# Kernel tuning notes

Hardware: AMD Instinct MI355X
Metric: run time of the kernel (lower is better)

The kernel has to match this reference:

```python
import jax, jax.numpy as jnp
import numpy as np

HEAD_SIZE = 64
EMBED = 512


def setup_inputs() -> dict:
    key = jax.random.key(0)
    kx, kk, kq, kv = jax.random.split(key, 4)
    x = jax.random.normal(kx, (4, 4096, EMBED), dtype=jnp.float32)
    # torch Linear(EMBED, HEAD_SIZE, bias=False) weight: [HEAD_SIZE, EMBED]
    scale = 1.0 / np.sqrt(EMBED)
    Wk = jax.random.normal(kk, (HEAD_SIZE, EMBED), dtype=jnp.float32) * scale
    Wq = jax.random.normal(kq, (HEAD_SIZE, EMBED), dtype=jnp.float32) * scale
    Wv = jax.random.normal(kv, (HEAD_SIZE, EMBED), dtype=jnp.float32) * scale
    return {"x": x, "Wk": Wk, "Wq": Wq, "Wv": Wv}


def reference(x, Wk, Wq, Wv):
    B, T, C = x.shape
    # projections: x @ W.T  -> [B, T, H]
    k = jnp.einsum('btc,hc->bth', x, Wk)
    q = jnp.einsum('btc,hc->bth', x, Wq)
    v = jnp.einsum('btc,hc->bth', x, Wv)
    # scores scaled by C**-0.5 (input embed dim, as in the source module)
    scores = jnp.einsum('bth,bsh->bts', q, k) * (C ** -0.5)  # [B, T, T]
    causal = jnp.tril(jnp.ones((T, T), dtype=bool))
    scores = jnp.where(causal, scores, -jnp.inf)
    weights = jax.nn.softmax(scores, axis=-1)
    # dropout p=0.0 -> identity
    out = jnp.einsum('bts,bsh->bth', weights, v)  # [B, T, H]
    return out
```

## Files before the change

kernel.cpp:

```cpp
#include <hip/hip_runtime.h>

typedef unsigned short u16;
typedef unsigned int   u32;

#define NB 4
#define NT 4096
#define NC 512
#define NH 64
#define ATT_SCALE 0.044194173824159216f
#define LOG2E     1.4426950408889634f
#define QSCALE    (ATT_SCALE * LOG2E)
#define NEG_BIG   -30000.0f
#define ITEMS3_PB 288

typedef __attribute__((ext_vector_type(8))) _Float16 half8;
typedef __attribute__((ext_vector_type(4))) _Float16 half4;
typedef __attribute__((ext_vector_type(4))) float    floatx4;

__device__ __forceinline__ void gload_lds16(const _Float16* g, _Float16* l) {
    __builtin_amdgcn_global_load_lds(
        (const __attribute__((address_space(1))) void*)g,
        (__attribute__((address_space(3))) void*)l, 16, 0, 0);
}


__global__ __launch_bounds__(256) void wconv(
    const float* __restrict__ Wk, const float* __restrict__ Wq,
    const float* __restrict__ Wv, _Float16* __restrict__ Wh)
{
    const int gid = blockIdx.x * 256 + threadIdx.x;
    const int w = gid >> 13;
    const int i = gid & 8191;
    const int h = i >> 7, c = (i & 127) * 4;
    const float* src = (w == 0) ? Wq : (w == 1) ? Wk : Wv;
    const float sc = (w == 0) ? QSCALE : 1.0f;
    float4 f = *(const float4*)&src[h * NC + c];
    half4 o = {(_Float16)(f.x * sc), (_Float16)(f.y * sc),
               (_Float16)(f.z * sc), (_Float16)(f.w * sc)};
    const int blk = ((w * 16 + (c >> 5)) * 4 + (h >> 4));
    *(half4*)&Wh[(size_t)blk * 512 + (h & 15) * 32 + ((c >> 3) & 3) * 8 + (c & 7)] = o;
}

__global__ __launch_bounds__(256) void qkv_mfma(
    const float* __restrict__ x, const _Float16* __restrict__ Wh,
    _Float16* __restrict__ Qf, _Float16* __restrict__ Kf,
    _Float16* __restrict__ Vf)
{
    __shared__ __align__(16) floatx4 red[3][12][64];

    const int tid  = threadIdx.x;
    const int wv   = tid >> 6;
    const int lane = tid & 63;
    const int quad = lane >> 4;
    const int id   = lane & 15;
    const int rowbase = blockIdx.x * 16;

    floatx4 acc[3][4] = {};
    const float* xp = x + (size_t)(rowbase + id) * NC + wv * 128;
    const int loff = id * 32 + quad * 8;

    float4 xr[8];
#pragma unroll
    for (int ksq = 0; ksq < 8; ++ksq)
        xr[ksq] = *(const float4*)&xp[(ksq >> 1) * 32 + quad * 8 + (ksq & 1) * 4];

#pragma unroll
    for (int ks = 0; ks < 4; ++ks) {
        float4 f0 = xr[2 * ks];
        float4 f1 = xr[2 * ks + 1];
        half8 a;
        a[0] = (_Float16)f0.x; a[1] = (_Float16)f0.y;
        a[2] = (_Float16)f0.z; a[3] = (_Float16)f0.w;
        a[4] = (_Float16)f1.x; a[5] = (_Float16)f1.y;
        a[6] = (_Float16)f1.z; a[7] = (_Float16)f1.w;
        const int ksg = wv * 4 + ks;
#pragma unroll
        for (int w = 0; w < 3; ++w)
#pragma unroll
            for (int nt = 0; nt < 4; ++nt) {
                half8 bf = *(const half8*)&Wh[(size_t)((w * 16 + ksg) * 4 + nt) * 512 + loff];
                acc[w][nt] = __builtin_amdgcn_mfma_f32_16x16x32_f16(a, bf, acc[w][nt], 0, 0, 0);
            }
    }

#pragma unroll
    for (int idx = 0; idx < 12; ++idx) {
        const int ow = idx / 3;
        if (ow != wv)
            red[(wv > ow) ? wv - 1 : wv][idx][lane] = acc[idx >> 2][idx & 3];
    }
    __syncthreads();

    const int b  = rowbase >> 12, L = rowbase & 4095;
    const int q16 = L >> 4, kt = L >> 6, tt = (L >> 4) & 3;
    const int kop = ((rowbase & 63) + quad * 4) >> 5;
    const int q4k = ((((rowbase & 63) + quad * 4) >> 3) & 3);

#define QKV_EPIL(IDX) do {                                                     \
    constexpr int w_ = (IDX) >> 2, nt_ = (IDX) & 3;                            \
    floatx4 a_ = acc[w_][nt_];                                                 \
    a_ += red[0][IDX][lane] + red[1][IDX][lane] + red[2][IDX][lane];           \
    if (w_ == 0 || w_ == 1) {                                                  \
        const int hop = nt_ >> 1;                                              \
        const int q4h = (nt_ * 2 + (id >> 3)) & 3;                             \
        const int j   = id & 7;                                                \
        const size_t ad = (w_ == 0)                                            \
            ? (size_t)((b * 256 + q16) * 2 + hop) * 512 + q4h * 8 + j          \
            : (size_t)(((b * 64 + kt) * 4 + tt) * 2 + hop) * 512 + q4h * 8 + j;\
        _Float16* dstp = (w_ == 0) ? Qf : Kf;                                  \
        _Pragma("unroll")                                                      \
        for (int r = 0; r < 4; ++r)                                            \
            dstp[ad + (quad * 4 + r) * 32] = (_Float16)a_[r];                  \
    } else {                                                                   \
        half4 vh = {(_Float16)a_[0], (_Float16)a_[1],                          \
                    (_Float16)a_[2], (_Float16)a_[3]};                         \
        const size_t va = (size_t)(((b * 64 + kt) * 4 + nt_) * 2 + kop) * 512  \
                        + id * 32 + q4k * 8 + (quad & 1) * 4;                  \
        *(half4*)&Vf[va] = vh;                                                 \
    }                                                                          \
} while (0)

    if (wv == 0)      { QKV_EPIL(0); QKV_EPIL(1);  QKV_EPIL(2);  }
    else if (wv == 1) { QKV_EPIL(3); QKV_EPIL(4);  QKV_EPIL(5);  }
    else if (wv == 2) { QKV_EPIL(6); QKV_EPIL(7);  QKV_EPIL(8);  }
    else              { QKV_EPIL(9); QKV_EPIL(10); QKV_EPIL(11); }
#undef QKV_EPIL
}

__global__ __launch_bounds__(256) void attn_part(
    const _Float16* __restrict__ Qf, const _Float16* __restrict__ Kf,
    const _Float16* __restrict__ Vf, _Float16* __restrict__ Opart,
    float2* __restrict__ MLpart)
{
    constexpr int KP = 72;
    __shared__ __align__(16) _Float16 KV[2][2][4096];
    __shared__ __align__(16) _Float16 Ps[4][16 * KP];

    const int tid  = threadIdx.x;
    const int wv   = tid >> 6;
    const int lane = tid & 63;
    const int quad = lane >> 4;
    const int id   = lane & 15;
    const int b    = blockIdx.y;
    const int item = (ITEMS3_PB - 1) - blockIdx.x;
    const int loff = id * 32 + quad * 8;

    int g = (int)(0.5f * (__builtin_sqrtf((float)item + 1.0f) - 1.0f));
    while (4 * (g + 1) * (g + 2) <= item) ++g;
    while (g > 0 && 4 * g * (g + 1) > item) --g;
    const int rem = item - 4 * g * (g + 1);
    const int np  = g + 1;
    const int qb  = 8 * g + rem / np;
    const int seg = rem - (rem / np) * np;
    const int ntl = qb + 1;
    const int t0 = seg * ntl / np, t1 = (seg + 1) * ntl / np;

    const size_t qa = (size_t)((b * 256 + qb * 4 + wv) * 2) * 512 + loff;
    const half8 qb0 = *(const half8*)&Qf[qa];
    const half8 qb1 = *(const half8*)&Qf[qa + 512];

    size_t gk = (size_t)((b * 64 + t0) * 8) * 512;
    const int c0 = 2 * wv, c1 = 2 * wv + 1;

    gload_lds16(&Kf[gk + (size_t)c0 * 512 + loff], &KV[0][0][c0 * 512]);
    gload_lds16(&Kf[gk + (size_t)c1 * 512 + loff], &KV[0][0][c1 * 512]);
    gload_lds16(&Vf[gk + (size_t)c0 * 512 + loff], &KV[0][1][c0 * 512]);
    gload_lds16(&Vf[gk + (size_t)c1 * 512 + loff], &KV[0][1][c1 * 512]);

    floatx4 o[4] = {};
    float m_i = NEG_BIG;
    float l_q = 0.f;

    asm volatile("s_waitcnt vmcnt(0)" ::: "memory");
    __syncthreads();

    int cur = 0;
    for (int kt = t0; kt < t1; ++kt) {
        const bool more = (kt + 1 < t1);
        if (more) {
            const size_t gn = gk + 4096;
            gload_lds16(&Kf[gn + (size_t)c0 * 512 + loff], &KV[cur ^ 1][0][c0 * 512]);
            gload_lds16(&Kf[gn + (size_t)c1 * 512 + loff], &KV[cur ^ 1][0][c1 * 512]);
            gload_lds16(&Vf[gn + (size_t)c0 * 512 + loff], &KV[cur ^ 1][1][c0 * 512]);
            gload_lds16(&Vf[gn + (size_t)c1 * 512 + loff], &KV[cur ^ 1][1][c1 * 512]);
        }
        const _Float16* Kc = &KV[cur][0][0];
        const _Float16* Vc = &KV[cur][1][0];

        floatx4 s4[4] = {};
#pragma unroll
        for (int t = 0; t < 4; ++t) {
            const half8 k0 = *(const half8*)&Kc[(size_t)(2 * t)     * 512 + lane * 8];
            const half8 k1 = *(const half8*)&Kc[(size_t)(2 * t + 1) * 512 + lane * 8];
            s4[t] = __builtin_amdgcn_mfma_f32_16x16x32_f16(k0, qb0, s4[t], 0, 0, 0);
            s4[t] = __builtin_amdgcn_mfma_f32_16x16x32_f16(k1, qb1, s4[t], 0, 0, 0);
        }

        if (kt == qb) {
            const int qrow = wv * 16 + id;
#pragma unroll
            for (int t = 0; t < 4; ++t)
#pragma unroll
                for (int r = 0; r < 4; ++r)
                    if (16 * t + quad * 4 + r > qrow)
                        s4[t][r] = NEG_BIG;
        }

        half8 vf[8];
#pragma unroll
        for (int c = 0; c < 8; ++c)
            vf[c] = *(const half8*)&Vc[(size_t)c * 512 + lane * 8];

        float pmax = s4[0][0];
#pragma unroll
        for (int t = 0; t < 4; ++t)
#pragma unroll
            for (int r = 0; r < 4; ++r) pmax = fmaxf(pmax, s4[t][r]);

        if (__any(pmax > m_i + 8.0f)) {
            float mx = pmax;
            mx = fmaxf(mx, __shfl_xor(mx, 16));
            mx = fmaxf(mx, __shfl_xor(mx, 32));
            const float mnew  = fmaxf(m_i, mx);
            const float alpha = exp2f(m_i - mnew);
            m_i = mnew;
            l_q *= alpha;
#pragma unroll
            for (int t = 0; t < 4; ++t)
#pragma unroll
                for (int r = 0; r < 4; ++r) o[t][r] *= alpha;
        }

        float psum = 0.f;
#pragma unroll
        for (int t = 0; t < 4; ++t)
#pragma unroll
            for (int r = 0; r < 4; ++r) {
                const float p = exp2f(s4[t][r] - m_i);
                s4[t][r] = p;
                psum += p;
            }
        l_q += psum;

#pragma unroll
        for (int t = 0; t < 4; ++t) {
            half4 ph = {(_Float16)s4[t][0], (_Float16)s4[t][1],
                        (_Float16)s4[t][2], (_Float16)s4[t][3]};
            *(half4*)&Ps[wv][id * KP + 16 * t + quad * 4] = ph;
        }
        const half8 pb0 = *(const half8*)&Ps[wv][id * KP + quad * 8];
        const half8 pb1 = *(const half8*)&Ps[wv][id * KP + 32 + quad * 8];

#pragma unroll
        for (int t = 0; t < 4; ++t) {
            o[t] = __builtin_amdgcn_mfma_f32_16x16x32_f16(vf[2 * t],     pb0, o[t], 0, 0, 0);
            o[t] = __builtin_amdgcn_mfma_f32_16x16x32_f16(vf[2 * t + 1], pb1, o[t], 0, 0, 0);
        }

        if (more)
            asm volatile("s_waitcnt vmcnt(0)" ::: "memory");
        __syncthreads();
        cur ^= 1;
        gk += 4096;
    }

    float l_t = l_q;
    l_t += __shfl_xor(l_t, 16);
    l_t += __shfl_xor(l_t, 32);

    const int p = b * ITEMS3_PB + item;
    const float rl = 1.f / l_t;
#pragma unroll
    for (int t = 0; t < 4; ++t) {
        half4 oh = {(_Float16)(o[t][0] * rl), (_Float16)(o[t][1] * rl),
                    (_Float16)(o[t][2] * rl), (_Float16)(o[t][3] * rl)};
        *(half4*)&Ps[wv][id * KP + 16 * t + quad * 4] = oh;
    }
    const int rr = lane >> 3, rc = (lane & 7) * 8;
    half8 u0 = *(const half8*)&Ps[wv][rr * KP + rc];
    half8 u1 = *(const half8*)&Ps[wv][(8 + rr) * KP + rc];
    _Float16* ob = &Opart[((size_t)p * 64 + wv * 16) * NH];
    *(half8*)&ob[rr * NH + rc] = u0;
    *(half8*)&ob[(8 + rr) * NH + rc] = u1;

    if (quad == 0)
        MLpart[(size_t)p * 64 + wv * 16 + id] = make_float2(m_i, l_t);
}

__global__ __launch_bounds__(256) void attn_combine(
    const _Float16* __restrict__ Opart, const float2* __restrict__ MLpart,
    float* __restrict__ out)
{
    const int b   = blockIdx.y;
    const int tid = threadIdx.x;
    const int row = blockIdx.x * 32 + (tid >> 3);
    const int hc  = tid & 7;
    const int qb  = row >> 6;
    const int rin = row & 63;
    const int g   = qb >> 3;
    const int m   = g + 1;
    const int base = 4 * g * (g + 1) + (qb & 7) * m;

    auto gidx = [&](int k) -> size_t {
        return ((size_t)b * ITEMS3_PB + base + k) * 64 + rin;
    };

    float2 ml[8];
#pragma unroll
    for (int k = 0; k < 8; ++k)
        ml[k] = MLpart[gidx(k < m ? k : 0)];

    half8 ohv[8];
#pragma unroll
    for (int k = 0; k < 8; ++k)
        ohv[k] = *(const half8*)&Opart[gidx(k < m ? k : 0) * NH + hc * 8];

    float M = NEG_BIG;
#pragma unroll
    for (int k = 0; k < 8; ++k)
        if (k < m) M = fmaxf(M, ml[k].x);

    float w[8], W = 0.f;
#pragma unroll
    for (int k = 0; k < 8; ++k) {
        const float wk = (k < m) ? ml[k].y * exp2f(ml[k].x - M) : 0.f;
        w[k] = wk; W += wk;
    }

    float acc[8] = {};
#pragma unroll
    for (int k = 0; k < 8; ++k)
#pragma unroll
        for (int j = 0; j < 8; ++j) acc[j] += w[k] * (float)ohv[k][j];

    const float rl = 1.f / W;
    float* dst = out + (size_t)(b * NT + row) * NH + hc * 8;
#pragma unroll
    for (int j = 0; j < 8; ++j) dst[j] = acc[j] * rl;
}

extern "C" void kernel_launch(void* const* d_in, const int* in_sizes, int n_in,
                              void* d_out, int out_size, void* d_ws, size_t ws_size,
                              hipStream_t stream) {
    const float* x  = (const float*)d_in[0];
    const float* Wk = (const float*)d_in[1];
    const float* Wq = (const float*)d_in[2];
    const float* Wv = (const float*)d_in[3];

    char* wsb = (char*)d_ws;
    _Float16* Qf    = (_Float16*)wsb;
    _Float16* Kf    = Qf + 1048576;
    _Float16* Vf    = Kf + 1048576;
    _Float16* Wh    = Vf + 1048576;
    float2*   MLpart= (float2*)(wsb + 6488064);
    _Float16* Opart = (_Float16*)(wsb + 7602176);

    wconv<<<96, 256, 0, stream>>>(Wk, Wq, Wv, Wh);
    qkv_mfma<<<1024, 256, 0, stream>>>(x, Wh, Qf, Kf, Vf);
    attn_part<<<dim3(ITEMS3_PB, NB), 256, 0, stream>>>(Qf, Kf, Vf, Opart, MLpart);
    attn_combine<<<dim3(128, NB), 256, 0, stream>>>(Opart, MLpart, (float*)d_out);
}
```

Baseline: 124.9 us.

## Restructure QKV projection to 64-row blocks with LDS pipelining; deepen attention prefetch

The QKV projection kernel now gives each block 64 rows, one 16-row slice per wave, and loops over all K-steps. Weight tiles and swizzled x tiles are streamed into LDS with async global-to-LDS loads, double-buffering the weights and triple-buffering x. This removes the cross-wave LDS reduction and cuts the grid to 256 blocks. The attention kernel moves to a prefetch distance of two tiles with partial vmcnt waits and raises wave priority around the MFMA sections, aiming to hide K/V load latency. The trade-off is fewer blocks for the projection, which may reduce occupancy, plus more complex waitcnt bookkeeping.

Result: no change. 122.5 us (median of 2 runs) (-1.9%).

```diff
diff --git a/kernel.cpp b/kernel.cpp
--- a/kernel.cpp
+++ b/kernel.cpp
@@ -17,7 +17,7 @@
 typedef __attribute__((ext_vector_type(4))) _Float16 half4;
 typedef __attribute__((ext_vector_type(4))) float    floatx4;
 
-__device__ __forceinline__ void gload_lds16(const _Float16* g, _Float16* l) {
+__device__ __forceinline__ void gld16(const void* g, void* l) {
     __builtin_amdgcn_global_load_lds(
         (const __attribute__((address_space(1))) void*)g,
         (__attribute__((address_space(3))) void*)l, 16, 0, 0);
@@ -46,85 +46,98 @@
     _Float16* __restrict__ Qf, _Float16* __restrict__ Kf,
     _Float16* __restrict__ Vf)
 {
-    __shared__ __align__(16) floatx4 red[3][12][64];
+    __shared__ __align__(16) _Float16 Ws[2][12 * 512];
+    __shared__ __align__(16) float    Xs[3][64 * 32];
 
     const int tid  = threadIdx.x;
     const int wv   = tid >> 6;
     const int lane = tid & 63;
     const int quad = lane >> 4;
     const int id   = lane & 15;
-    const int rowbase = blockIdx.x * 16;
+    const int loff = id * 32 + quad * 8;
+    const int rowbase = blockIdx.x * 64;
+
+    const int xrow  = wv * 16 + (lane >> 3);
+    const int xchk  = (lane & 7) ^ ((lane >> 3) & 7);
+    const float* xs0 = x + (size_t)(rowbase + xrow) * NC + xchk * 4;
+    const float* xs1 = xs0 + 8 * NC;
 
     floatx4 acc[3][4] = {};
-    const float* xp = x + (size_t)(rowbase + id) * NC + wv * 128;
-    const int loff = id * 32 + quad * 8;
-
-    float4 xr[8];
-#pragma unroll
-    for (int ksq = 0; ksq < 8; ++ksq)
-        xr[ksq] = *(const float4*)&xp[(ksq >> 1) * 32 + quad * 8 + (ksq & 1) * 4];
-
-#pragma unroll
-    for (int ks = 0; ks < 4; ++ks) {
-        float4 f0 = xr[2 * ks];
-        float4 f1 = xr[2 * ks + 1];
+
+    gld16(xs0, &Xs[0][wv * 512]);
+    gld16(xs1, &Xs[0][wv * 512 + 256]);
+#pragma unroll
+    for (int jj = 0; jj < 3; ++jj) {
+        const int f = 3 * wv + jj;
+        gld16(Wh + (size_t)(((f >> 2) * 16 + 0) * 4 + (f & 3)) * 512 + loff,
+              &Ws[0][f * 512]);
+    }
+    gld16(xs0 + 32, &Xs[1][wv * 512]);
+    gld16(xs1 + 32, &Xs[1][wv * 512 + 256]);
+
+    int xcur = 0;
+    for (int s = 0; s < 16; ++s) {
+        if (s + 2 < 16) asm volatile("s_waitcnt vmcnt(2)" ::: "memory");
+        else            asm volatile("s_waitcnt vmcnt(0)" ::: "memory");
+        __syncthreads();
+
+        if (s + 1 < 16) {
+            _Float16* wdst = &Ws[(s + 1) & 1][0];
+#pragma unroll
+            for (int jj = 0; jj < 3; ++jj) {
+                const int f = 3 * wv + jj;
+                gld16(Wh + (size_t)(((f >> 2) * 16 + (s + 1)) * 4 + (f & 3)) * 512 + loff,
+                      wdst + f * 512);
+            }
+        }
+        if (s + 2 < 16) {
+            const int nb = (xcur + 2 >= 3) ? xcur - 1 : xcur + 2;
+            float* xdst = &Xs[nb][wv * 512];
+            gld16(xs0 + (s + 2) * 32, xdst);
+            gld16(xs1 + (s + 2) * 32, xdst + 256);
+        }
+
+        const float* Xc = &Xs[xcur][wv * 512 + id * 32];
+        float4 f0 = *(const float4*)&Xc[((quad * 2 + 0) ^ (id & 7)) << 2];
+        float4 f1 = *(const float4*)&Xc[((quad * 2 + 1) ^ (id & 7)) << 2];
         half8 a;
         a[0] = (_Float16)f0.x; a[1] = (_Float16)f0.y;
         a[2] = (_Float16)f0.z; a[3] = (_Float16)f0.w;
         a[4] = (_Float16)f1.x; a[5] = (_Float16)f1.y;
         a[6] = (_Float16)f1.z; a[7] = (_Float16)f1.w;
-        const int ksg = wv * 4 + ks;
-#pragma unroll
-        for (int w = 0; w < 3; ++w)
-#pragma unroll
-            for (int nt = 0; nt < 4; ++nt) {
-                half8 bf = *(const half8*)&Wh[(size_t)((w * 16 + ksg) * 4 + nt) * 512 + loff];
-                acc[w][nt] = __builtin_amdgcn_mfma_f32_16x16x32_f16(a, bf, acc[w][nt], 0, 0, 0);
-            }
-    }
-
-#pragma unroll
-    for (int idx = 0; idx < 12; ++idx) {
-        const int ow = idx / 3;
-        if (ow != wv)
-            red[(wv > ow) ? wv - 1 : wv][idx][lane] = acc[idx >> 2][idx & 3];
-    }
-    __syncthreads();
-
-    const int b  = rowbase >> 12, L = rowbase & 4095;
-    const int q16 = L >> 4, kt = L >> 6, tt = (L >> 4) & 3;
-    const int kop = ((rowbase & 63) + quad * 4) >> 5;
-    const int q4k = ((((rowbase & 63) + quad * 4) >> 3) & 3);
-
-#define QKV_EPIL(IDX) do {                                                     \
-    constexpr int w_ = (IDX) >> 2, nt_ = (IDX) & 3;                            \
-    floatx4 a_ = acc[w_][nt_];                                                 \
-    a_ += red[0][IDX][lane] + red[1][IDX][lane] + red[2][IDX][lane];           \
-    if (w_ == 0 || w_ == 1) {                                                  \
-        const int hop = nt_ >> 1;                                              \
-        const int q4h = (nt_ * 2 + (id >> 3)) & 3;                             \
-        const int j   = id & 7;                                                \
-        const size_t ad = (w_ == 0)                                            \
-            ? (size_t)((b * 256 + q16) * 2 + hop) * 512 + q4h * 8 + j          \
-            : (size_t)(((b * 64 + kt) * 4 + tt) * 2 + hop) * 512 + q4h * 8 + j;\
-        _Float16* dstp = (w_ == 0) ? Qf : Kf;                                  \
-        _Pragma("unroll")                                                      \
-        for (int r = 0; r < 4; ++r)                                            \
-            dstp[ad + (quad * 4 + r) * 32] = (_Float16)a_[r];                  \
-    } else {                                                                   \
-        half4 vh = {(_Float16)a_[0], (_Float16)a_[1],                          \
-                    (_Float16)a_[2], (_Float16)a_[3]};                         \
-        const size_t va = (size_t)(((b * 64 + kt) * 4 + nt_) * 2 + kop) * 512  \
-                        + id * 32 + q4k * 8 + (quad & 1) * 4;                  \
-        *(half4*)&Vf[va] = vh;                                                 \
-    }                                                                          \
-} while (0)
-
-    if (wv == 0)      { QKV_EPIL(0); QKV_EPIL(1);  QKV_EPIL(2);  }
-    else if (wv == 1) { QKV_EPIL(3); QKV_EPIL(4);  QKV_EPIL(5);  }
-    else if (wv == 2) { QKV_EPIL(6); QKV_EPIL(7);  QKV_EPIL(8);  }
-    else              { QKV_EPIL(9); QKV_EPIL(10); QKV_EPIL(11); }
-#undef QKV_EPIL
+
+        const _Float16* Wc = &Ws[s & 1][0];
+#pragma unroll
+        for (int f = 0; f < 12; ++f) {
+            half8 bf = *(const half8*)&Wc[f * 512 + lane * 8];
+            acc[f >> 2][f & 3] = __builtin_amdgcn_mfma_f32_16x16x32_f16(a, bf, acc[f >> 2][f & 3], 0, 0, 0);
+        }
+        xcur = (xcur + 1 == 3) ? 0 : xcur + 1;
+    }
+
+    const int rowb = rowbase + wv * 16;
+    const int b2 = rowb >> 12, L = rowb & 4095;
+    const int q16 = L >> 4, ktt = L >> 6, tt = (L >> 4) & 3;
+    const int kop = ((rowb & 63) + quad * 4) >> 5;
+    const int q4k = (((rowb & 63) + quad * 4) >> 3) & 3;
+#pragma unroll
+    for (int nt = 0; nt < 4; ++nt) {
+        const int hop = nt >> 1;
+        const int q4h = (nt * 2 + (id >> 3)) & 3;
+        const int j   = id & 7;
+        const size_t qa2 = (size_t)((b2 * 256 + q16) * 2 + hop) * 512 + q4h * 8 + j;
+        const size_t ka2 = (size_t)(((b2 * 64 + ktt) * 4 + tt) * 2 + hop) * 512 + q4h * 8 + j;
+#pragma unroll
+        for (int r = 0; r < 4; ++r) {
+            Qf[qa2 + (quad * 4 + r) * 32] = (_Float16)acc[0][nt][r];
+            Kf[ka2 + (quad * 4 + r) * 32] = (_Float16)acc[1][nt][r];
+        }
+        half4 vh = {(_Float16)acc[2][nt][0], (_Float16)acc[2][nt][1],
+                    (_Float16)acc[2][nt][2], (_Float16)acc[2][nt][3]};
+        const size_t va2 = (size_t)(((b2 * 64 + ktt) * 4 + nt) * 2 + kop) * 512
+                         + id * 32 + q4k * 8 + (quad & 1) * 4;
+        *(half4*)&Vf[va2] = vh;
+    }
 }
 
 __global__ __launch_bounds__(256) void attn_part(
@@ -162,32 +175,31 @@
     size_t gk = (size_t)((b * 64 + t0) * 8) * 512;
     const int c0 = 2 * wv, c1 = 2 * wv + 1;
 
-    gload_lds16(&Kf[gk + (size_t)c0 * 512 + loff], &KV[0][0][c0 * 512]);
-    gload_lds16(&Kf[gk + (size_t)c1 * 512 + loff], &KV[0][0][c1 * 512]);
-    gload_lds16(&Vf[gk + (size_t)c0 * 512 + loff], &KV[0][1][c0 * 512]);
-    gload_lds16(&Vf[gk + (size_t)c1 * 512 + loff], &KV[0][1][c1 * 512]);
+#define STAGE4(GBASE, BUF) do {                                              \
+    gld16(&Kf[(GBASE) + (size_t)c0 * 512 + loff], &KV[BUF][0][c0 * 512]);    \
+    gld16(&Kf[(GBASE) + (size_t)c1 * 512 + loff], &KV[BUF][0][c1 * 512]);    \
+    gld16(&Vf[(GBASE) + (size_t)c0 * 512 + loff], &KV[BUF][1][c0 * 512]);    \
+    gld16(&Vf[(GBASE) + (size_t)c1 * 512 + loff], &KV[BUF][1][c1 * 512]);    \
+} while (0)
+
+    STAGE4(gk, 0);
+    if (t0 + 1 < t1) STAGE4(gk + 4096, 1);
 
     floatx4 o[4] = {};
     float m_i = NEG_BIG;
     float l_q = 0.f;
 
-    asm volatile("s_waitcnt vmcnt(0)" ::: "memory");
-    __syncthreads();
-
     int cur = 0;
     for (int kt = t0; kt < t1; ++kt) {
-        const bool more = (kt + 1 < t1);
-        if (more) {
-            const size_t gn = gk + 4096;
-            gload_lds16(&Kf[gn + (size_t)c0 * 512 + loff], &KV[cur ^ 1][0][c0 * 512]);
-            gload_lds16(&Kf[gn + (size_t)c1 * 512 + loff], &KV[cur ^ 1][0][c1 * 512]);
-            gload_lds16(&Vf[gn + (size_t)c0 * 512 + loff], &KV[cur ^ 1][1][c0 * 512]);
-            gload_lds16(&Vf[gn + (size_t)c1 * 512 + loff], &KV[cur ^ 1][1][c1 * 512]);
-        }
+        if (kt + 1 < t1) asm volatile("s_waitcnt vmcnt(4)" ::: "memory");
+        else             asm volatile("s_waitcnt vmcnt(0)" ::: "memory");
+        __syncthreads();
+
         const _Float16* Kc = &KV[cur][0][0];
         const _Float16* Vc = &KV[cur][1][0];
 
         floatx4 s4[4] = {};
+        __builtin_amdgcn_s_setprio(1);
 #pragma unroll
         for (int t = 0; t < 4; ++t) {
             const half8 k0 = *(const half8*)&Kc[(size_t)(2 * t)     * 512 + lane * 8];
@@ -195,6 +207,7 @@
             s4[t] = __builtin_amdgcn_mfma_f32_16x16x32_f16(k0, qb0, s4[t], 0, 0, 0);
             s4[t] = __builtin_amdgcn_mfma_f32_16x16x32_f16(k1, qb1, s4[t], 0, 0, 0);
         }
+        __builtin_amdgcn_s_setprio(0);
 
         if (kt == qb) {
             const int qrow = wv * 16 + id;
@@ -251,18 +264,21 @@
         const half8 pb0 = *(const half8*)&Ps[wv][id * KP + quad * 8];
         const half8 pb1 = *(const half8*)&Ps[wv][id * KP + 32 + quad * 8];
 
+        __builtin_amdgcn_s_setprio(1);
 #pragma unroll
         for (int t = 0; t < 4; ++t) {
             o[t] = __builtin_amdgcn_mfma_f32_16x16x32_f16(vf[2 * t],     pb0, o[t], 0, 0, 0);
             o[t] = __builtin_amdgcn_mfma_f32_16x16x32_f16(vf[2 * t + 1], pb1, o[t], 0, 0, 0);
         }
-
-        if (more)
-            asm volatile("s_waitcnt vmcnt(0)" ::: "memory");
+        __builtin_amdgcn_s_setprio(0);
+
         __syncthreads();
+        if (kt + 2 < t1)
+            STAGE4(gk + 2 * 4096, cur);
         cur ^= 1;
         gk += 4096;
     }
+#undef STAGE4
 
     float l_t = l_q;
     l_t += __shfl_xor(l_t, 16);
@@ -356,7 +372,7 @@
     _Float16* Opart = (_Float16*)(wsb + 7602176);
 
     wconv<<<96, 256, 0, stream>>>(Wk, Wq, Wv, Wh);
-    qkv_mfma<<<1024, 256, 0, stream>>>(x, Wh, Qf, Kf, Vf);
+    qkv_mfma<<<256, 256, 0, stream>>>(x, Wh, Qf, Kf, Vf);
     attn_part<<<dim3(ITEMS3_PB, NB), 256, 0, stream>>>(Qf, Kf, Vf, Opart, MLpart);
     attn_combine<<<dim3(128, NB), 256, 0, stream>>>(Opart, MLpart, (float*)d_out);
 }
```
